# Optimization experiments

Measured on AMD Instinct MI355X. Metric: run time of the kernel, lower is better.

The kernel has to match this reference:

```python
import jax, jax.numpy as jnp
import numpy as np

D = 2048  # input_size
H = 2048  # hidden_size
K = 4096  # number of children


def setup_inputs() -> dict:
    key = jax.random.key(0)
    ks = jax.random.split(key, 12)
    sD = 1.0 / np.sqrt(D)
    sH = 1.0 / np.sqrt(H)
    return {
        "input": jax.random.normal(ks[0], (D,), dtype=jnp.float32),
        "children_c": jax.random.normal(ks[1], (K, H), dtype=jnp.float32),
        "children_h": jax.random.normal(ks[2], (K, H), dtype=jnp.float32),
        "W_iou_x": jax.random.uniform(ks[3], (3 * H, D), jnp.float32, -sD, sD),
        "b_iou_x": jax.random.uniform(ks[4], (3 * H,), jnp.float32, -sD, sD),
        "W_iou_h": jax.random.uniform(ks[5], (3 * H, H), jnp.float32, -sH, sH),
        "b_iou_h": jax.random.uniform(ks[6], (3 * H,), jnp.float32, -sH, sH),
        "W_fx": jax.random.uniform(ks[7], (H, D), jnp.float32, -sD, sD),
        "b_fx": jax.random.uniform(ks[8], (H,), jnp.float32, -sD, sD),
        "W_fh": jax.random.uniform(ks[9], (H, H), jnp.float32, -sH, sH),
        "b_fh": jax.random.uniform(ks[10], (H,), jnp.float32, -sH, sH),
    }


def reference(input, children_c, children_h,
              W_iou_x, b_iou_x, W_iou_h, b_iou_h,
              W_fx, b_fx, W_fh, b_fh):
    # iou = iou_x(input) + iou_h(sum_k h_k)  -> [3H]
    h_sum = jnp.sum(children_h, axis=0)
    iou = (W_iou_x @ input + b_iou_x) + (W_iou_h @ h_sum + b_iou_h)
    i, o, u = jnp.split(iou, 3)
    i = jax.nn.sigmoid(i)
    o = jax.nn.sigmoid(o)
    u = jnp.tanh(u)
    # per-child forget gates, batched over K (original loops in Python):
    # f_k = sigmoid(f_x(input) + f_h(h_k))  -> [K, H]
    fx = W_fx @ input + b_fx                       # [H], computed once
    fh = children_h @ W_fh.T + b_fh                # [K, H] GEMM
    f = jax.nn.sigmoid(fx[None, :] + fh)           # [K, H]
    c = i * u + jnp.sum(f * children_c, axis=0)    # [H]
    h = o * jnp.tanh(c)                            # [H]
    return (o, c, h)
```

## Files before the change

kernel.cpp:

```cpp
#include <hip/hip_runtime.h>

typedef unsigned short u16;
typedef short bf16x8 __attribute__((ext_vector_type(8)));
typedef float f32x4 __attribute__((ext_vector_type(4)));

#define D_IN 2048
#define H_DIM 2048
#define K_CH 4096

__device__ __forceinline__ u16 f2bf(float f) {
  unsigned int u = __float_as_uint(f);
  u += 0x7fffu + ((u >> 16) & 1u);
  return (u16)(u >> 16);
}
__device__ __forceinline__ float sigmoidf(float x) {
  return 1.0f / (1.0f + __expf(-x));
}
__device__ __forceinline__ uint4 packrow(float4 a, float4 b) {
  uint4 w;
  w.x = (unsigned)f2bf(a.x) | ((unsigned)f2bf(a.y) << 16);
  w.y = (unsigned)f2bf(a.z) | ((unsigned)f2bf(a.w) << 16);
  w.z = (unsigned)f2bf(b.x) | ((unsigned)f2bf(b.y) << 16);
  w.w = (unsigned)f2bf(b.z) | ((unsigned)f2bf(b.w) << 16);
  return w;
}

__global__ __launch_bounds__(256) void k1(
    const float* __restrict__ ch, const float* __restrict__ wfh,
    const float* __restrict__ Wfx, const float* __restrict__ bfx,
    const float* __restrict__ bfh, const float* __restrict__ x,
    float* __restrict__ partials, u16* __restrict__ chb,
    u16* __restrict__ wfhb, float* __restrict__ g,
    float* __restrict__ hsum, float* __restrict__ accv) {
  const int t = threadIdx.x;
  const int bid = blockIdx.x;
  if (bid < 1024) {
    const int r0 = bid * 4;
    float4 a[4], b[4];
#pragma unroll
    for (int r = 0; r < 4; ++r) {
      const float4* p = (const float4*)(ch + (size_t)(r0 + r) * H_DIM + t * 8);
      a[r] = p[0];
      b[r] = p[1];
    }
    float s0 = 0.f, s1 = 0.f, s2 = 0.f, s3 = 0.f;
    float s4 = 0.f, s5 = 0.f, s6 = 0.f, s7 = 0.f;
#pragma unroll
    for (int r = 0; r < 4; ++r) {
      s0 += a[r].x; s1 += a[r].y; s2 += a[r].z; s3 += a[r].w;
      s4 += b[r].x; s5 += b[r].y; s6 += b[r].z; s7 += b[r].w;
      *(uint4*)(chb + (size_t)(r0 + r) * H_DIM + t * 8) = packrow(a[r], b[r]);
    }
    float4 lo, hi;
    lo.x = s0; lo.y = s1; lo.z = s2; lo.w = s3;
    hi.x = s4; hi.y = s5; hi.z = s6; hi.w = s7;
    float* pp = partials + (size_t)bid * H_DIM + t * 8;
    *(float4*)pp = lo;
    *(float4*)(pp + 4) = hi;
  } else if (bid < 1536) {
    const size_t base = (size_t)(bid - 1024) * 8192 + t * 8;
    float4 a[4], b[4];
#pragma unroll
    for (int j = 0; j < 4; ++j) {
      const float4* p = (const float4*)(wfh + base + j * 2048);
      a[j] = p[0];
      b[j] = p[1];
    }
#pragma unroll
    for (int j = 0; j < 4; ++j)
      *(uint4*)(wfhb + base + j * 2048) = packrow(a[j], b[j]);
  } else if (bid < 2048) {
    const int wave = t >> 6, lane = t & 63;
    const int h = (bid - 1536) * 4 + wave;
    const float4* w = (const float4*)(Wfx + (size_t)h * D_IN);
    const float4* xv = (const float4*)x;
    float s = 0.f;
#pragma unroll
    for (int i = 0; i < 8; ++i) {
      int idx = i * 64 + lane;
      float4 av = w[idx], bv = xv[idx];
      s += av.x * bv.x + av.y * bv.y + av.z * bv.z + av.w * bv.w;
    }
#pragma unroll
    for (int off = 32; off > 0; off >>= 1) s += __shfl_xor(s, off);
    if (lane == 0) g[h] = s + bfx[h] + bfh[h];
  } else {
    float4 z = {0.f, 0.f, 0.f, 0.f};
    ((float4*)hsum)[t * 2] = z;
    ((float4*)hsum)[t * 2 + 1] = z;
    ((float4*)accv)[t * 2] = z;
    ((float4*)accv)[t * 2 + 1] = z;
  }
}

__global__ __launch_bounds__(256) void kred(const float* __restrict__ partials,
                                            float* __restrict__ hsum) {
  const int c = blockIdx.x * 256 + threadIdx.x;
  const int p0 = blockIdx.y * 128;
  float a0 = 0.f, a1 = 0.f, a2 = 0.f, a3 = 0.f;
  float a4 = 0.f, a5 = 0.f, a6 = 0.f, a7 = 0.f;
  for (int p = p0; p < p0 + 128; p += 8) {
    a0 += partials[(size_t)(p + 0) * H_DIM + c];
    a1 += partials[(size_t)(p + 1) * H_DIM + c];
    a2 += partials[(size_t)(p + 2) * H_DIM + c];
    a3 += partials[(size_t)(p + 3) * H_DIM + c];
    a4 += partials[(size_t)(p + 4) * H_DIM + c];
    a5 += partials[(size_t)(p + 5) * H_DIM + c];
    a6 += partials[(size_t)(p + 6) * H_DIM + c];
    a7 += partials[(size_t)(p + 7) * H_DIM + c];
  }
  float s = ((a0 + a1) + (a2 + a3)) + ((a4 + a5) + (a6 + a7));
  atomicAdd(hsum + c, s);
}

#define BM 128
#define BN 128
#define BK 64

__global__ __launch_bounds__(256) void k3(
    const u16* __restrict__ chb, const float* __restrict__ cc,
    const u16* __restrict__ wfhb, const float* __restrict__ g,
    float* __restrict__ accv, const float* __restrict__ Wix,
    const float* __restrict__ bix, const float* __restrict__ Wih,
    const float* __restrict__ bih, const float* __restrict__ x,
    const float* __restrict__ hsum, float* __restrict__ iou) {
  __shared__ u16 As[BM * BK];
  __shared__ u16 Bs[BN * BK];

  const int bid = blockIdx.x;
  const int t = threadIdx.x;
  const int wave = t >> 6, lane = t & 63;

  if (bid < 512) {
    const int lrow = lane & 15, lquad = lane >> 4;
    const int wm = wave >> 1, wn = wave & 1;
    const int row0 = (bid & 31) * BM;
    const int col0 = (bid >> 5) * BN;

    f32x4 acc[4][4] = {};

    const int srow = lane >> 3;
    const int schunk = (lane & 7) ^ srow;
    const u16* agbase = chb  + (size_t)(row0 + wave * 32 + srow) * H_DIM + schunk * 8;
    const u16* bgbase = wfhb + (size_t)(col0 + wave * 32 + srow) * H_DIM + schunk * 8;

    for (int kb = 0; kb < D_IN / BK; ++kb) {
      __syncthreads();
#pragma unroll
      for (int i = 0; i < 4; ++i)
        __builtin_amdgcn_global_load_lds(
            (const __attribute__((address_space(1))) void*)(agbase + (size_t)i * 8 * H_DIM + kb * BK),
            (__attribute__((address_space(3))) void*)(As + (wave * 32 + i * 8) * 64),
            16, 0, 0);
#pragma unroll
      for (int i = 0; i < 4; ++i)
        __builtin_amdgcn_global_load_lds(
            (const __attribute__((address_space(1))) void*)(bgbase + (size_t)i * 8 * H_DIM + kb * BK),
            (__attribute__((address_space(3))) void*)(Bs + (wave * 32 + i * 8) * 64),
            16, 0, 0);
      __syncthreads();

#pragma unroll
      for (int step = 0; step < 2; ++step) {
        const int slot = ((step * 4 + lquad) ^ (lrow & 7)) * 8;
        bf16x8 fa[4], fb[4];
#pragma unroll
        for (int i = 0; i < 4; ++i)
          fa[i] = *(const bf16x8*)(As + (wm * 64 + i * 16 + lrow) * 64 + slot);
#pragma unroll
        for (int i = 0; i < 4; ++i)
          fb[i] = *(const bf16x8*)(Bs + (wn * 64 + i * 16 + lrow) * 64 + slot);
#pragma unroll
        for (int mi = 0; mi < 4; ++mi)
#pragma unroll
          for (int ni = 0; ni < 4; ++ni)
            acc[mi][ni] = __builtin_amdgcn_mfma_f32_16x16x32_bf16(
                fa[mi], fb[ni], acc[mi][ni], 0, 0, 0);
      }
    }

#pragma unroll
    for (int ni = 0; ni < 4; ++ni) {
      const int colg = col0 + wn * 64 + ni * 16 + lrow;
      const float gv = g[colg];
      float s = 0.f;
#pragma unroll
      for (int mi = 0; mi < 4; ++mi) {
        const int rowg = row0 + wm * 64 + mi * 16 + lquad * 4;
#pragma unroll
        for (int r = 0; r < 4; ++r) {
          float f = sigmoidf(gv + acc[mi][ni][r]);
          s += f * cc[(size_t)(rowg + r) * H_DIM + colg];
        }
      }
      s += __shfl_xor(s, 16);
      s += __shfl_xor(s, 32);
      if (lquad == 0) atomicAdd(accv + colg, s);
    }
  } else {
    const int row = (bid - 512) * 4 + wave;
    const float4* wx = (const float4*)(Wix + (size_t)row * D_IN);
    const float4* wh = (const float4*)(Wih + (size_t)row * H_DIM);
    const float4* xv = (const float4*)x;
    const float4* hv = (const float4*)hsum;
    float s = 0.f;
#pragma unroll
    for (int i = 0; i < 8; ++i) {
      int idx = i * 64 + lane;
      float4 a = wx[idx], b = xv[idx];
      s += a.x * b.x + a.y * b.y + a.z * b.z + a.w * b.w;
      float4 c = wh[idx], d = hv[idx];
      s += c.x * d.x + c.y * d.y + c.z * d.z + c.w * d.w;
    }
#pragma unroll
    for (int off = 32; off > 0; off >>= 1) s += __shfl_xor(s, off);
    if (lane == 0) iou[row] = s + bix[row] + bih[row];
  }
}

__global__ __launch_bounds__(256) void kfinal(const float* __restrict__ iou,
                                              const float* __restrict__ accv,
                                              float* __restrict__ out) {
  const int h = blockIdx.x * 256 + threadIdx.x;
  float si = sigmoidf(iou[h]);
  float so = sigmoidf(iou[H_DIM + h]);
  float tu = tanhf(iou[2 * H_DIM + h]);
  float c = si * tu + accv[h];
  float hh = so * tanhf(c);
  out[h] = so;
  out[H_DIM + h] = c;
  out[2 * H_DIM + h] = hh;
}

extern "C" void kernel_launch(void* const* d_in, const int* in_sizes, int n_in,
                              void* d_out, int out_size, void* d_ws, size_t ws_size,
                              hipStream_t stream) {
  const float* x   = (const float*)d_in[0];
  const float* cc  = (const float*)d_in[1];
  const float* ch  = (const float*)d_in[2];
  const float* Wix = (const float*)d_in[3];
  const float* bix = (const float*)d_in[4];
  const float* Wih = (const float*)d_in[5];
  const float* bih = (const float*)d_in[6];
  const float* Wfx = (const float*)d_in[7];
  const float* bfx = (const float*)d_in[8];
  const float* Wfh = (const float*)d_in[9];
  const float* bfh = (const float*)d_in[10];

  float* ws   = (float*)d_ws;
  float* hsum = ws;
  float* iou  = ws + 2048;
  float* g    = ws + 8192;
  float* accv = ws + 10240;
  float* partials = ws + 12288;
  u16* chb  = (u16*)(ws + 12288 + 1024 * 2048);
  u16* wfhb = chb + (size_t)K_CH * H_DIM;
  float* out = (float*)d_out;

  k1<<<2049, 256, 0, stream>>>(ch, Wfh, Wfx, bfx, bfh, x, partials, chb, wfhb, g, hsum, accv);
  kred<<<dim3(8, 8), 256, 0, stream>>>(partials, hsum);
  k3<<<2048, 256, 0, stream>>>(chb, cc, wfhb, g, accv, Wix, bix, Wih, bih, x, hsum, iou);
  kfinal<<<8, 256, 0, stream>>>(iou, accv, out);
}
```

Baseline: 271.8 us.

## Double-buffer GEMM LDS stages and reschedule matvecs across kernels

```diff
diff --git a/kernel.cpp b/kernel.cpp
--- a/kernel.cpp
+++ b/kernel.cpp
@@ -29,9 +29,11 @@
     const float* __restrict__ ch, const float* __restrict__ wfh,
     const float* __restrict__ Wfx, const float* __restrict__ bfx,
     const float* __restrict__ bfh, const float* __restrict__ x,
-    float* __restrict__ partials, u16* __restrict__ chb,
-    u16* __restrict__ wfhb, float* __restrict__ g,
-    float* __restrict__ hsum, float* __restrict__ accv) {
+    const float* __restrict__ Wix, const float* __restrict__ bix,
+    const float* __restrict__ bih, float* __restrict__ partials,
+    u16* __restrict__ chb, u16* __restrict__ wfhb, float* __restrict__ g,
+    float* __restrict__ ioux, float* __restrict__ hsum,
+    float* __restrict__ accv) {
   const int t = threadIdx.x;
   const int bid = blockIdx.x;
   if (bid < 1024) {
@@ -84,6 +86,21 @@
 #pragma unroll
     for (int off = 32; off > 0; off >>= 1) s += __shfl_xor(s, off);
     if (lane == 0) g[h] = s + bfx[h] + bfh[h];
+  } else if (bid < 3584) {
+    const int wave = t >> 6, lane = t & 63;
+    const int row = (bid - 2048) * 4 + wave;
+    const float4* w = (const float4*)(Wix + (size_t)row * D_IN);
+    const float4* xv = (const float4*)x;
+    float s = 0.f;
+#pragma unroll
+    for (int i = 0; i < 8; ++i) {
+      int idx = i * 64 + lane;
+      float4 av = w[idx], bv = xv[idx];
+      s += av.x * bv.x + av.y * bv.y + av.z * bv.z + av.w * bv.w;
+    }
+#pragma unroll
+    for (int off = 32; off > 0; off >>= 1) s += __shfl_xor(s, off);
+    if (lane == 0) ioux[row] = s + bix[row] + bih[row];
   } else {
     float4 z = {0.f, 0.f, 0.f, 0.f};
     ((float4*)hsum)[t * 2] = z;
@@ -93,129 +110,142 @@
   }
 }
 
-__global__ __launch_bounds__(256) void kred(const float* __restrict__ partials,
-                                            float* __restrict__ hsum) {
-  const int c = blockIdx.x * 256 + threadIdx.x;
-  const int p0 = blockIdx.y * 128;
-  float a0 = 0.f, a1 = 0.f, a2 = 0.f, a3 = 0.f;
-  float a4 = 0.f, a5 = 0.f, a6 = 0.f, a7 = 0.f;
-  for (int p = p0; p < p0 + 128; p += 8) {
-    a0 += partials[(size_t)(p + 0) * H_DIM + c];
-    a1 += partials[(size_t)(p + 1) * H_DIM + c];
-    a2 += partials[(size_t)(p + 2) * H_DIM + c];
-    a3 += partials[(size_t)(p + 3) * H_DIM + c];
-    a4 += partials[(size_t)(p + 4) * H_DIM + c];
-    a5 += partials[(size_t)(p + 5) * H_DIM + c];
-    a6 += partials[(size_t)(p + 6) * H_DIM + c];
-    a7 += partials[(size_t)(p + 7) * H_DIM + c];
-  }
-  float s = ((a0 + a1) + (a2 + a3)) + ((a4 + a5) + (a6 + a7));
-  atomicAdd(hsum + c, s);
-}
-
 #define BM 128
 #define BN 128
 #define BK 64
 
-__global__ __launch_bounds__(256) void k3(
+__global__ __launch_bounds__(256) void kG(
     const u16* __restrict__ chb, const float* __restrict__ cc,
     const u16* __restrict__ wfhb, const float* __restrict__ g,
-    float* __restrict__ accv, const float* __restrict__ Wix,
-    const float* __restrict__ bix, const float* __restrict__ Wih,
-    const float* __restrict__ bih, const float* __restrict__ x,
-    const float* __restrict__ hsum, float* __restrict__ iou) {
-  __shared__ u16 As[BM * BK];
-  __shared__ u16 Bs[BN * BK];
+    const float* __restrict__ partials, float* __restrict__ hsum,
+    float* __restrict__ accv) {
+  __shared__ u16 As[2][BM * BK];
+  __shared__ u16 Bs[2][BN * BK];
 
   const int bid = blockIdx.x;
   const int t = threadIdx.x;
+
+  if (bid < 64) {
+    const int c = (bid & 7) * 256 + t;
+    const int p0 = (bid >> 3) * 128;
+    float a0 = 0.f, a1 = 0.f, a2 = 0.f, a3 = 0.f;
+    float a4 = 0.f, a5 = 0.f, a6 = 0.f, a7 = 0.f;
+    for (int p = p0; p < p0 + 128; p += 8) {
+      a0 += partials[(size_t)(p + 0) * H_DIM + c];
+      a1 += partials[(size_t)(p + 1) * H_DIM + c];
+      a2 += partials[(size_t)(p + 2) * H_DIM + c];
+      a3 += partials[(size_t)(p + 3) * H_DIM + c];
+      a4 += partials[(size_t)(p + 4) * H_DIM + c];
+      a5 += partials[(size_t)(p + 5) * H_DIM + c];
+      a6 += partials[(size_t)(p + 6) * H_DIM + c];
+      a7 += partials[(size_t)(p + 7) * H_DIM + c];
+    }
+    float s = ((a0 + a1) + (a2 + a3)) + ((a4 + a5) + (a6 + a7));
+    atomicAdd(hsum + c, s);
+    return;
+  }
+
+  const int gb = bid - 64;
   const int wave = t >> 6, lane = t & 63;
-
-  if (bid < 512) {
-    const int lrow = lane & 15, lquad = lane >> 4;
-    const int wm = wave >> 1, wn = wave & 1;
-    const int row0 = (bid & 31) * BM;
-    const int col0 = (bid >> 5) * BN;
-
-    f32x4 acc[4][4] = {};
-
-    const int srow = lane >> 3;
-    const int schunk = (lane & 7) ^ srow;
-    const u16* agbase = chb  + (size_t)(row0 + wave * 32 + srow) * H_DIM + schunk * 8;
-    const u16* bgbase = wfhb + (size_t)(col0 + wave * 32 + srow) * H_DIM + schunk * 8;
-
-    for (int kb = 0; kb < D_IN / BK; ++kb) {
-      __syncthreads();
-#pragma unroll
-      for (int i = 0; i < 4; ++i)
-        __builtin_amdgcn_global_load_lds(
-            (const __attribute__((address_space(1))) void*)(agbase + (size_t)i * 8 * H_DIM + kb * BK),
-            (__attribute__((address_space(3))) void*)(As + (wave * 32 + i * 8) * 64),
-            16, 0, 0);
-#pragma unroll
-      for (int i = 0; i < 4; ++i)
-        __builtin_amdgcn_global_load_lds(
-            (const __attribute__((address_space(1))) void*)(bgbase + (size_t)i * 8 * H_DIM + kb * BK),
-            (__attribute__((address_space(3))) void*)(Bs + (wave * 32 + i * 8) * 64),
-            16, 0, 0);
-      __syncthreads();
-
-#pragma unroll
-      for (int step = 0; step < 2; ++step) {
-        const int slot = ((step * 4 + lquad) ^ (lrow & 7)) * 8;
-        bf16x8 fa[4], fb[4];
-#pragma unroll
-        for (int i = 0; i < 4; ++i)
-          fa[i] = *(const bf16x8*)(As + (wm * 64 + i * 16 + lrow) * 64 + slot);
-#pragma unroll
-        for (int i = 0; i < 4; ++i)
-          fb[i] = *(const bf16x8*)(Bs + (wn * 64 + i * 16 + lrow) * 64 + slot);
-#pragma unroll
-        for (int mi = 0; mi < 4; ++mi)
-#pragma unroll
-          for (int ni = 0; ni < 4; ++ni)
-            acc[mi][ni] = __builtin_amdgcn_mfma_f32_16x16x32_bf16(
-                fa[mi], fb[ni], acc[mi][ni], 0, 0, 0);
+  const int lrow = lane & 15, lquad = lane >> 4;
+  const int wm = wave >> 1, wn = wave & 1;
+  const int row0 = (gb & 31) * BM;
+  const int col0 = (gb >> 5) * BN;
+
+  f32x4 acc[4][4] = {};
+
+  const int srow = lane >> 3;
+  const int schunk = (lane & 7) ^ srow;
+  const u16* agbase = chb  + (size_t)(row0 + wave * 32 + srow) * H_DIM + schunk * 8;
+  const u16* bgbase = wfhb + (size_t)(col0 + wave * 32 + srow) * H_DIM + schunk * 8;
+
+#define STAGE(buf, kb)                                                        \
+  do {                                                                        \
+    _Pragma("unroll")                                                         \
+    for (int i = 0; i < 4; ++i)                                               \
+      __builtin_amdgcn_global_load_lds(                                       \
+          (const __attribute__((address_space(1))) void*)(agbase + (size_t)i * 8 * H_DIM + (kb) * BK), \
+          (__attribute__((address_space(3))) void*)(&As[buf][(wave * 32 + i * 8) * 64]), \
+          16, 0, 0);                                                          \
+    _Pragma("unroll")                                                         \
+    for (int i = 0; i < 4; ++i)                                               \
+      __builtin_amdgcn_global_load_lds(                                       \
+          (const __attribute__((address_space(1))) void*)(bgbase + (size_t)i * 8 * H_DIM + (kb) * BK), \
+          (__attribute__((address_space(3))) void*)(&Bs[buf][(wave * 32 + i * 8) * 64]), \
+          16, 0, 0);                                                          \
+  } while (0)
+
+#define COMPUTE(buf)                                                          \
+  do {                                                                        \
+    _Pragma("unroll")                                                         \
+    for (int step = 0; step < 2; ++step) {                                    \
+      const int slot = ((step * 4 + lquad) ^ (lrow & 7)) * 8;                 \
+      bf16x8 fa[4], fb[4];                                                    \
+      _Pragma("unroll")                                                       \
+      for (int i = 0; i < 4; ++i)                                             \
+        fa[i] = *(const bf16x8*)(&As[buf][(wm * 64 + i * 16 + lrow) * 64 + slot]); \
+      _Pragma("unroll")                                                       \
+      for (int i = 0; i < 4; ++i)                                             \
+        fb[i] = *(const bf16x8*)(&Bs[buf][(wn * 64 + i * 16 + lrow) * 64 + slot]); \
+      _Pragma("unroll")                                                       \
+      for (int mi = 0; mi < 4; ++mi)                                          \
+        _Pragma("unroll")                                                     \
+        for (int ni = 0; ni < 4; ++ni)                                        \
+          acc[mi][ni] = __builtin_amdgcn_mfma_f32_16x16x32_bf16(              \
+              fa[mi], fb[ni], acc[mi][ni], 0, 0, 0);                          \
+    }                                                                         \
+  } while (0)
+
+  STAGE(0, 0);
+  __syncthreads();
+
+  for (int kb = 0; kb < D_IN / BK - 1; ++kb) {
+    const int cur = kb & 1;
+    STAGE(cur ^ 1, kb + 1);
+    COMPUTE(cur);
+    __syncthreads();
+  }
+  COMPUTE(1);
+
+#pragma unroll
+  for (int ni = 0; ni < 4; ++ni) {
+    const int colg = col0 + wn * 64 + ni * 16 + lrow;
+    const float gv = g[colg];
+    float s = 0.f;
+#pragma unroll
+    for (int mi = 0; mi < 4; ++mi) {
+      const int rowg = row0 + wm * 64 + mi * 16 + lquad * 4;
+#pragma unroll
+      for (int r = 0; r < 4; ++r) {
+        float f = sigmoidf(gv + acc[mi][ni][r]);
+        s += f * cc[(size_t)(rowg + r) * H_DIM + colg];
       }
     }
-
-#pragma unroll
-    for (int ni = 0; ni < 4; ++ni) {
-      const int colg = col0 + wn * 64 + ni * 16 + lrow;
-      const float gv = g[colg];
-      float s = 0.f;
-#pragma unroll
-      for (int mi = 0; mi < 4; ++mi) {
-        const int rowg = row0 + wm * 64 + mi * 16 + lquad * 4;
-#pragma unroll
-        for (int r = 0; r < 4; ++r) {
-          float f = sigmoidf(gv + acc[mi][ni][r]);
-          s += f * cc[(size_t)(rowg + r) * H_DIM + colg];
-        }
-      }
-      s += __shfl_xor(s, 16);
-      s += __shfl_xor(s, 32);
-      if (lquad == 0) atomicAdd(accv + colg, s);
-    }
-  } else {
-    const int row = (bid - 512) * 4 + wave;
-    const float4* wx = (const float4*)(Wix + (size_t)row * D_IN);
-    const float4* wh = (const float4*)(Wih + (size_t)row * H_DIM);
-    const float4* xv = (const float4*)x;
-    const float4* hv = (const float4*)hsum;
-    float s = 0.f;
-#pragma unroll
-    for (int i = 0; i < 8; ++i) {
-      int idx = i * 64 + lane;
-      float4 a = wx[idx], b = xv[idx];
-      s += a.x * b.x + a.y * b.y + a.z * b.z + a.w * b.w;
-      float4 c = wh[idx], d = hv[idx];
-      s += c.x * d.x + c.y * d.y + c.z * d.z + c.w * d.w;
-    }
-#pragma unroll
-    for (int off = 32; off > 0; off >>= 1) s += __shfl_xor(s, off);
-    if (lane == 0) iou[row] = s + bix[row] + bih[row];
-  }
+    s += __shfl_xor(s, 16);
+    s += __shfl_xor(s, 32);
+    if (lquad == 0) atomicAdd(accv + colg, s);
+  }
+#undef STAGE
+#undef COMPUTE
+}
+
+__global__ __launch_bounds__(256) void kmv2(const float* __restrict__ Wih,
+                                            const float* __restrict__ hsum,
+                                            float* __restrict__ iou) {
+  const int wave = threadIdx.x >> 6, lane = threadIdx.x & 63;
+  const int row = blockIdx.x * 4 + wave;
+  const float4* w = (const float4*)(Wih + (size_t)row * H_DIM);
+  const float4* hv = (const float4*)hsum;
+  float s = 0.f;
+#pragma unroll
+  for (int i = 0; i < 8; ++i) {
+    int idx = i * 64 + lane;
+    float4 a = w[idx], b = hv[idx];
+    s += a.x * b.x + a.y * b.y + a.z * b.z + a.w * b.w;
+  }
+#pragma unroll
+  for (int off = 32; off > 0; off >>= 1) s += __shfl_xor(s, off);
+  if (lane == 0) iou[row] += s;
 }
 
 __global__ __launch_bounds__(256) void kfinal(const float* __restrict__ iou,
@@ -257,8 +287,9 @@
   u16* wfhb = chb + (size_t)K_CH * H_DIM;
   float* out = (float*)d_out;
 
-  k1<<<2049, 256, 0, stream>>>(ch, Wfh, Wfx, bfx, bfh, x, partials, chb, wfhb, g, hsum, accv);
-  kred<<<dim3(8, 8), 256, 0, stream>>>(partials, hsum);
-  k3<<<2048, 256, 0, stream>>>(chb, cc, wfhb, g, accv, Wix, bix, Wih, bih, x, hsum, iou);
+  k1<<<3585, 256, 0, stream>>>(ch, Wfh, Wfx, bfx, bfh, x, Wix, bix, bih,
+                               partials, chb, wfhb, g, iou, hsum, accv);
+  kG<<<576, 256, 0, stream>>>(chb, cc, wfhb, g, partials, hsum, accv);
+  kmv2<<<1536, 256, 0, stream>>>(Wih, hsum, iou);
   kfinal<<<8, 256, 0, stream>>>(iou, accv, out);
 }
```

After: 264.7 us. -2.6%, faster.
